# Kernel tuning notes

Measured on AMD Instinct MI355X. Metric: run time of the kernel, lower is better.

## Reference

```python
import jax, jax.numpy as jnp
import numpy as np

B = 1024
N_CPGS = 20000
N_FREQS = N_CPGS // 2 + 1  # 10001
HIDDEN = (256, 128, 64)
LN_EPS = 1e-5


def setup_inputs() -> dict:
    key = jax.random.key(0)
    keys = jax.random.split(key, 16)
    inp = {"x": jax.random.normal(keys[0], (B, N_CPGS), dtype=jnp.float32)}
    in_dim = N_FREQS
    for i, h in enumerate(HIDDEN):
        inp[f"W{i}"] = jax.random.normal(keys[1 + i], (h, in_dim), dtype=jnp.float32) * 0.01
        inp[f"alpha{i}"] = jnp.full((h, in_dim), 0.01, dtype=jnp.float32)
        inp[f"b{i}"] = jnp.zeros((h,), dtype=jnp.float32)
        inp[f"eta{i}"] = jnp.asarray(0.1, dtype=jnp.float32)
        inp[f"g{i}"] = jnp.ones((h,), dtype=jnp.float32)   # LayerNorm gamma
        inp[f"be{i}"] = jnp.zeros((h,), dtype=jnp.float32)  # LayerNorm beta
        in_dim = h
    inp["head_w"] = jax.random.normal(keys[10], (1, in_dim), dtype=jnp.float32) * (1.0 / np.sqrt(in_dim))
    inp["head_b"] = jnp.zeros((1,), dtype=jnp.float32)
    return inp


def _hebbian_layer(x, W, alpha, b, eta):
    # y_slow = x W^T + b;  plastic[b,i] = eta * tanh(y_slow)[b,i] * sum_j sigmoid(alpha)[i,j] * x_norm[b,j] * x[b,j]
    y_slow = jnp.einsum('bd,hd->bh', x, W) + b
    x_norm = x / (jnp.linalg.norm(x, axis=-1, keepdims=True) + 1e-8)
    c = x_norm * x  # (B, in) -- collapses the (B,out,in) outer-product trace algebraically
    plastic = eta * jnp.tanh(y_slow) * jnp.einsum('bd,hd->bh', c, jax.nn.sigmoid(alpha))
    return y_slow + plastic


def _layer_norm(h, g, be):
    mu = jnp.mean(h, axis=-1, keepdims=True)
    var = jnp.mean((h - mu) ** 2, axis=-1, keepdims=True)
    return (h - mu) * jax.lax.rsqrt(var + LN_EPS) * g + be


def reference(x, W0, alpha0, b0, eta0, g0, be0,
              W1, alpha1, b1, eta1, g1, be1,
              W2, alpha2, b2, eta2, g2, be2,
              head_w, head_b):
    # FFT spectral front-end
    xc = x - jnp.mean(x, axis=1, keepdims=True)
    h = jnp.log1p(jnp.abs(jnp.fft.rfft(xc, axis=1)))  # (B, N_FREQS)
    params = [(W0, alpha0, b0, eta0, g0, be0),
              (W1, alpha1, b1, eta1, g1, be1),
              (W2, alpha2, b2, eta2, g2, be2)]
    for (W, a, b, eta, g, be) in params:
        h = jax.nn.gelu(_layer_norm(_hebbian_layer(h, W, a, b, eta), g, be), approximate=False)
        # dropout is identity in eval mode
    return (jnp.einsum('bd,od->bo', h, head_w) + head_b)[:, 0]  # (B,)
```

## Files before the change

kernel.cpp:

```cpp
#include <hip/hip_runtime.h>
#include <hip/hip_bf16.h>
#include <math.h>

typedef short bf16x8 __attribute__((ext_vector_type(8)));
typedef float f32x4 __attribute__((ext_vector_type(4)));

static __device__ __forceinline__ unsigned short f2bf(float f) {
    unsigned int u = __float_as_uint(f);
    unsigned int r = (u + 0x7fffu + ((u >> 16) & 1u)) >> 16;
    return (unsigned short)r;
}

static __device__ __forceinline__ float gelu_f(float x) {
    return 0.5f * x * (1.f + erff(x * 0.70710678118654752f));
}

static __device__ __forceinline__ void gload_lds16(const void* g, void* l) {
    __builtin_amdgcn_global_load_lds(
        (const __attribute__((address_space(1))) unsigned int*)g,
        (__attribute__((address_space(3))) unsigned int*)l, 16, 0, 0);
}

static __device__ __forceinline__ int ldsmap(int i) { return i + (i >> 6); }

static __device__ __forceinline__ int rev4(int k) {
    int d0 = k % 10; k /= 10;
    int d1 = k % 10; k /= 10;
    int d2 = k % 10; int d3 = k / 10;
    return d0 * 1000 + d1 * 100 + d2 * 10 + d3;
}

static __device__ __forceinline__ void dft5(
    float a0r, float a0i, float a1r, float a1i, float a2r, float a2i,
    float a3r, float a3i, float a4r, float a4i,
    float* Xr, float* Xi)
{
    const float c1 = 0.30901699437494742f, c2 = -0.80901699437494745f;
    const float s1 = 0.95105651629515357f, s2 = 0.58778525229247312f;
    float t1r = a1r + a4r, t1i = a1i + a4i;
    float d1r = a1r - a4r, d1i = a1i - a4i;
    float t2r = a2r + a3r, t2i = a2i + a3i;
    float d2r = a2r - a3r, d2i = a2i - a3i;
    Xr[0] = a0r + t1r + t2r; Xi[0] = a0i + t1i + t2i;
    float m1r = a0r + c1 * t1r + c2 * t2r, m1i = a0i + c1 * t1i + c2 * t2i;
    float m2r = a0r + c2 * t1r + c1 * t2r, m2i = a0i + c2 * t1i + c1 * t2i;
    float n1r = s1 * d1r + s2 * d2r, n1i = s1 * d1i + s2 * d2i;
    float n2r = s2 * d1r - s1 * d2r, n2i = s2 * d1i - s1 * d2i;
    Xr[1] = m1r + n1i; Xi[1] = m1i - n1r;
    Xr[4] = m1r - n1i; Xi[4] = m1i + n1r;
    Xr[2] = m2r + n2i; Xi[2] = m2i - n2r;
    Xr[3] = m2r - n2i; Xi[3] = m2i + n2r;
}

__global__ __launch_bounds__(512, 4)
void fft_kernel(const float* __restrict__ x,
                unsigned short* __restrict__ hb,
                unsigned short* __restrict__ cb)
{
    __shared__ float reb[10156];
    __shared__ float imb[10156];
    __shared__ float redbuf[8];

    const int b = blockIdx.x;
    const int tid = threadIdx.x;
    const int lane = tid & 63;
    const int wv = tid >> 6;
    const float* xr = x + (size_t)b * 20000;

    float sum = 0.f;
    for (int i4 = tid; i4 < 5000; i4 += 512) {
        float4 v = ((const float4*)xr)[i4];
        sum += v.x + v.y + v.z + v.w;
        int n = i4 * 2;
        reb[ldsmap(n)]     = v.x; imb[ldsmap(n)]     = v.y;
        reb[ldsmap(n + 1)] = v.z; imb[ldsmap(n + 1)] = v.w;
    }
    #pragma unroll
    for (int o = 32; o; o >>= 1) sum += __shfl_xor(sum, o);
    __syncthreads();
    if (lane == 0) redbuf[wv] = sum;
    __syncthreads();
    float tot = 0.f;
    #pragma unroll
    for (int i = 0; i < 8; ++i) tot += redbuf[i];
    const float mean = tot * (1.f / 20000.f);

    const float WR[5] = {1.f, 0.80901699437494745f, 0.30901699437494742f,
                         -0.30901699437494742f, -0.80901699437494745f};
    const float WI[5] = {0.f, -0.58778525229247312f, -0.95105651629515357f,
                         -0.95105651629515357f, -0.58778525229247312f};

    #pragma unroll
    for (int s = 0; s < 4; ++s) {
        const int L  = (s == 0) ? 1000 : (s == 1) ? 100 : (s == 2) ? 10 : 1;
        const int sc = (s == 0) ? 1 : (s == 1) ? 10 : (s == 2) ? 100 : 1000;
        const float mm = (s == 0) ? mean : 0.f;
        for (int w = tid; w < 1000; w += 512) {
            const int g = w / L;
            const int j = w - g * L;
            const int base = g * (10 * L) + j;
            float ar[10], ai[10];
            #pragma unroll
            for (int u = 0; u < 10; ++u) {
                int idx = ldsmap(base + u * L);
                ar[u] = reb[idx] - mm;
                ai[u] = imb[idx] - mm;
            }
            float Er[5], Ei[5], Or[5], Oi[5];
            dft5(ar[0], ai[0], ar[2], ai[2], ar[4], ai[4], ar[6], ai[6], ar[8], ai[8], Er, Ei);
            dft5(ar[1], ai[1], ar[3], ai[3], ar[5], ai[5], ar[7], ai[7], ar[9], ai[9], Or, Oi);
            #pragma unroll
            for (int k = 1; k < 5; ++k) {
                float tr = Or[k] * WR[k] - Oi[k] * WI[k];
                Oi[k] = Or[k] * WI[k] + Oi[k] * WR[k];
                Or[k] = tr;
            }
            const float ang = (float)(j * sc) * -6.28318530717958648e-4f;
            float w1c, w1s;
            __sincosf(ang, &w1s, &w1c);
            float twr[10], twi[10];
            twr[0] = 1.f; twi[0] = 0.f;
            #pragma unroll
            for (int t = 1; t < 10; ++t) {
                twr[t] = twr[t - 1] * w1c - twi[t - 1] * w1s;
                twi[t] = twr[t - 1] * w1s + twi[t - 1] * w1c;
            }
            #pragma unroll
            for (int k = 0; k < 5; ++k) {
                float xr0 = Er[k] + Or[k], xi0 = Ei[k] + Oi[k];
                float xr1 = Er[k] - Or[k], xi1 = Ei[k] - Oi[k];
                int i0 = ldsmap(base + k * L);
                int i1 = ldsmap(base + (k + 5) * L);
                if (k == 0) {
                    reb[i0] = xr0;
                    imb[i0] = xi0;
                } else {
                    reb[i0] = xr0 * twr[k] - xi0 * twi[k];
                    imb[i0] = xr0 * twi[k] + xi0 * twr[k];
                }
                reb[i1] = xr1 * twr[k + 5] - xi1 * twi[k + 5];
                imb[i1] = xr1 * twi[k + 5] + xi1 * twr[k + 5];
            }
        }
        __syncthreads();
    }

    float harr[20];
    float sumsq = 0.f;
    unsigned short* hrow = hb + (size_t)b * 10240;
    #pragma unroll
    for (int i = 0; i < 20; ++i) {
        int k = tid + i * 512;
        float hval = 0.f;
        if (k <= 10000) {
            int k1 = (k == 10000) ? 0 : k;
            int k2 = (10000 - k) % 10000;
            int i1 = ldsmap(rev4(k1));
            int i2 = ldsmap(rev4(k2));
            float zr = reb[i1], zi = imb[i1];
            float wr = reb[i2], wi = imb[i2];
            float er = 0.5f * (zr + wr);
            float ei = 0.5f * (zi - wi);
            float odr = 0.5f * (zi + wi);
            float odi = -0.5f * (zr - wr);
            float ct, st;
            __sincosf((float)k * -3.14159265358979324e-4f, &st, &ct);
            float xre = er + ct * odr - st * odi;
            float xim = ei + ct * odi + st * odr;
            hval = log1pf(sqrtf(xre * xre + xim * xim));
        }
        harr[i] = hval;
        hrow[k] = f2bf(hval);
        sumsq += hval * hval;
    }
    #pragma unroll
    for (int o = 32; o; o >>= 1) sumsq += __shfl_xor(sumsq, o);
    __syncthreads();
    if (lane == 0) redbuf[wv] = sumsq;
    __syncthreads();
    float tsq = 0.f;
    #pragma unroll
    for (int i = 0; i < 8; ++i) tsq += redbuf[i];
    const float inv = 1.f / (sqrtf(tsq) + 1e-8f);

    unsigned short* crow = cb + (size_t)b * 10240;
    #pragma unroll
    for (int i = 0; i < 20; ++i) {
        int k = tid + i * 512;
        crow[k] = f2bf(harr[i] * harr[i] * inv);
    }
}

__global__ __launch_bounds__(256)
void prep_kernel(const float* __restrict__ W0, const float* __restrict__ A0,
                 unsigned short* __restrict__ Wb, unsigned short* __restrict__ Sb,
                 const float* __restrict__ W1, const float* __restrict__ A1,
                 const float* __restrict__ W2, const float* __restrict__ A2,
                 float* __restrict__ W1T, float* __restrict__ S1T,
                 float* __restrict__ W2T, float* __restrict__ S2T)
{
    int idx = blockIdx.x * 256 + threadIdx.x;
    if (idx < 1280128) {
        const bool isW = idx < 640064;
        const int f4 = isW ? idx : idx - 640064;
        const float* src = isW ? W0 : A0;
        unsigned short* dst = isW ? Wb : Sb;
        float4 v = ((const float4*)src)[f4];
        float e[4] = {v.x, v.y, v.z, v.w};
        int flat = f4 * 4;
        int row = flat / 10001;
        int col = flat - row * 10001;
        #pragma unroll
        for (int i = 0; i < 4; ++i) {
            if (col == 10001) { row++; col = 0; }
            float val = isW ? e[i] : 1.f / (1.f + expf(-e[i]));
            dst[(size_t)row * 10240 + col] = f2bf(val);
            col++;
        }
    } else if (idx < 1341312) {
        int i = idx - 1280128;
        int row = i / 239;
        int col = 10001 + (i - row * 239);
        Wb[(size_t)row * 10240 + col] = 0;
        Sb[(size_t)row * 10240 + col] = 0;
    } else if (idx < 1423232) {
        int o = idx - 1341312;
        if (o < 32768) {
            int d = o >> 7, h = o & 127;
            W1T[o] = W1[h * 256 + d];
        } else if (o < 65536) {
            int p = o - 32768;
            int d = p >> 7, h = p & 127;
            S1T[p] = 1.f / (1.f + expf(-A1[h * 256 + d]));
        } else if (o < 73728) {
            int p = o - 65536;
            int d = p >> 6, h = p & 63;
            W2T[p] = W2[h * 128 + d];
        } else {
            int p = o - 73728;
            int d = p >> 6, h = p & 63;
            S2T[p] = 1.f / (1.f + expf(-A2[h * 128 + d]));
        }
    }
}

__global__ __launch_bounds__(256, 2)
void gemm0_kernel(const unsigned short* __restrict__ hb, const unsigned short* __restrict__ cb,
                  const unsigned short* __restrict__ Wb, const unsigned short* __restrict__ Sb,
                  float* __restrict__ Py, float* __restrict__ Pp)
{
    __shared__ unsigned short Ah[128 * 64];
    __shared__ unsigned short Ac[128 * 64];
    __shared__ unsigned short Bw[64 * 64];
    __shared__ unsigned short Bs[64 * 64];

    const int t = threadIdx.x;
    const int b0 = blockIdx.x * 128;
    const int n0 = blockIdx.y * 64;
    const int z = blockIdx.z;
    const int lane = t & 63;
    const int wv = t >> 6;
    const int ml = lane & 15;
    const int q4 = lane >> 4;
    const int s0 = q4 ^ (ml & 7);

    const int sub = lane >> 3;
    const int sl = lane & 7;
    const int gsw = sl ^ sub;

    f32x4 accY[2][4], accP[2][4];
    #pragma unroll
    for (int mt = 0; mt < 2; ++mt)
        #pragma unroll
        for (int nt = 0; nt < 4; ++nt) {
            accY[mt][nt] = (f32x4){0.f, 0.f, 0.f, 0.f};
            accP[mt][nt] = (f32x4){0.f, 0.f, 0.f, 0.f};
        }

    const int kbase = z * 640;

    for (int step = 0; step < 10; ++step) {
        const int k0 = kbase + step * 64;
        __syncthreads();
        #pragma unroll
        for (int j = 0; j < 4; ++j) {
            const int c = wv * 4 + j;
            const size_t go = (size_t)(b0 + c * 8 + sub) * 10240 + k0 + gsw * 8;
            gload_lds16(&hb[go], &Ah[c * 512]);
            gload_lds16(&cb[go], &Ac[c * 512]);
        }
        #pragma unroll
        for (int j = 0; j < 2; ++j) {
            const int c = wv * 2 + j;
            const size_t go = (size_t)(n0 + c * 8 + sub) * 10240 + k0 + gsw * 8;
            gload_lds16(&Wb[go], &Bw[c * 512]);
            gload_lds16(&Sb[go], &Bs[c * 512]);
        }
        __syncthreads();

        #pragma unroll
        for (int kk = 0; kk < 2; ++kk) {
            const int slot = (s0 ^ (kk << 2)) << 3;
            bf16x8 ah[2], ac[2], bw[4], bs[4];
            #pragma unroll
            for (int mt = 0; mt < 2; ++mt) {
                int mrow = wv * 32 + mt * 16 + ml;
                ah[mt] = *(const bf16x8*)&Ah[mrow * 64 + slot];
                ac[mt] = *(const bf16x8*)&Ac[mrow * 64 + slot];
            }
            #pragma unroll
            for (int nt = 0; nt < 4; ++nt) {
                int nrow = nt * 16 + ml;
                bw[nt] = *(const bf16x8*)&Bw[nrow * 64 + slot];
                bs[nt] = *(const bf16x8*)&Bs[nrow * 64 + slot];
            }
            #pragma unroll
            for (int mt = 0; mt < 2; ++mt)
                #pragma unroll
                for (int nt = 0; nt < 4; ++nt) {
                    accY[mt][nt] = __builtin_amdgcn_mfma_f32_16x16x32_bf16(ah[mt], bw[nt], accY[mt][nt], 0, 0, 0);
                    accP[mt][nt] = __builtin_amdgcn_mfma_f32_16x16x32_bf16(ac[mt], bs[nt], accP[mt][nt], 0, 0, 0);
                }
        }
    }

    const int rq = q4 * 4;
    #pragma unroll
    for (int mt = 0; mt < 2; ++mt)
        #pragma unroll
        for (int nt = 0; nt < 4; ++nt)
            #pragma unroll
            for (int r = 0; r < 4; ++r) {
                int m = b0 + wv * 32 + mt * 16 + rq + r;
                int n = n0 + nt * 16 + ml;
                size_t o = ((size_t)z * 1024 + m) * 256 + n;
                Py[o] = accY[mt][nt][r];
                Pp[o] = accP[mt][nt][r];
            }
}

__global__ __launch_bounds__(256)
void combine0_kernel(const float* __restrict__ Py, const float* __restrict__ Pp,
                     const float* __restrict__ b0v, const float* __restrict__ eta0p,
                     const float* __restrict__ g0, const float* __restrict__ be0,
                     float* __restrict__ h1, float* __restrict__ c1)
{
    __shared__ float red[4];
    const int b = blockIdx.x;
    const int h = threadIdx.x;
    const int lane = h & 63;
    const int wv = h >> 6;

    float ys = 0.f, ps = 0.f;
    for (int s = 0; s < 16; ++s) {
        size_t o = ((size_t)s * 1024 + b) * 256 + h;
        ys += Py[o];
        ps += Pp[o];
    }
    float y = ys + b0v[h];
    float v = y + eta0p[0] * tanhf(y) * ps;

    float s1 = v;
    #pragma unroll
    for (int o = 32; o; o >>= 1) s1 += __shfl_xor(s1, o);
    __syncthreads();
    if (lane == 0) red[wv] = s1;
    __syncthreads();
    float sum = red[0] + red[1] + red[2] + red[3];

    float s2 = v * v;
    #pragma unroll
    for (int o = 32; o; o >>= 1) s2 += __shfl_xor(s2, o);
    __syncthreads();
    if (lane == 0) red[wv] = s2;
    __syncthreads();
    float sumsq = red[0] + red[1] + red[2] + red[3];

    float mu = sum * (1.f / 256.f);
    float var = sumsq * (1.f / 256.f) - mu * mu;
    float u = (v - mu) * rsqrtf(var + 1e-5f) * g0[h] + be0[h];
    float gl = gelu_f(u);

    float s3 = gl * gl;
    #pragma unroll
    for (int o = 32; o; o >>= 1) s3 += __shfl_xor(s3, o);
    __syncthreads();
    if (lane == 0) red[wv] = s3;
    __syncthreads();
    float gsq = red[0] + red[1] + red[2] + red[3];
    float inv = 1.f / (sqrtf(gsq) + 1e-8f);

    h1[(size_t)b * 256 + h] = gl;
    c1[(size_t)b * 256 + h] = gl * gl * inv;
}

__global__ __launch_bounds__(256)
void tail_kernel(const float* __restrict__ h1, const float* __restrict__ c1,
                 const float* __restrict__ W1T, const float* __restrict__ S1T,
                 const float* __restrict__ b1, const float* __restrict__ eta1p,
                 const float* __restrict__ g1, const float* __restrict__ be1,
                 const float* __restrict__ W2T, const float* __restrict__ S2T,
                 const float* __restrict__ b2, const float* __restrict__ eta2p,
                 const float* __restrict__ g2, const float* __restrict__ be2,
                 const float* __restrict__ hw, const float* __restrict__ hbod,
                 float* __restrict__ out)
{
    __shared__ float sh[8][256];
    __shared__ float sc[8][256];
    __shared__ float sv[8][128];
    __shared__ float sh2[8][128];
    __shared__ float sc2[8][128];
    __shared__ float sv2[8][64];

    const int t = threadIdx.x;
    const int b0 = blockIdx.x * 8;
    const int lane = t & 63;
    const int wv = t >> 6;

    #pragma unroll
    for (int i = 0; i < 8; ++i) {
        int idx = t + i * 256;
        int r = idx >> 8, d = idx & 255;
        sh[r][d] = h1[(size_t)(b0 + r) * 256 + d];
        sc[r][d] = c1[(size_t)(b0 + r) * 256 + d];
    }
    __syncthreads();

    const int hcol = t & 127;
    const int r2 = t >> 7;
    float ya[4] = {0.f, 0.f, 0.f, 0.f};
    float pa[4] = {0.f, 0.f, 0.f, 0.f};
    for (int d = 0; d < 256; ++d) {
        float w = W1T[d * 128 + hcol];
        float s = S1T[d * 128 + hcol];
        #pragma unroll
        for (int i = 0; i < 4; ++i) {
            int r = r2 * 4 + i;
            ya[i] += sh[r][d] * w;
            pa[i] += sc[r][d] * s;
        }
    }
    const float e1 = eta1p[0];
    #pragma unroll
    for (int i = 0; i < 4; ++i) {
        int r = r2 * 4 + i;
        float y = ya[i] + b1[hcol];
        sv[r][hcol] = y + e1 * tanhf(y) * pa[i];
    }
    __syncthreads();

    #pragma unroll
    for (int rr = 0; rr < 2; ++rr) {
        int r = wv * 2 + rr;
        float v0 = sv[r][lane];
        float v1 = sv[r][lane + 64];
        float s = v0 + v1, sq = v0 * v0 + v1 * v1;
        #pragma unroll
        for (int o = 32; o; o >>= 1) { s += __shfl_xor(s, o); sq += __shfl_xor(sq, o); }
        float mu = s * (1.f / 128.f);
        float var = sq * (1.f / 128.f) - mu * mu;
        float rs = rsqrtf(var + 1e-5f);
        float u0 = (v0 - mu) * rs * g1[lane] + be1[lane];
        float u1 = (v1 - mu) * rs * g1[lane + 64] + be1[lane + 64];
        float ge0 = gelu_f(u0);
        float ge1 = gelu_f(u1);
        float gsq = ge0 * ge0 + ge1 * ge1;
        #pragma unroll
        for (int o = 32; o; o >>= 1) gsq += __shfl_xor(gsq, o);
        float inv = 1.f / (sqrtf(gsq) + 1e-8f);
        sh2[r][lane] = ge0; sh2[r][lane + 64] = ge1;
        sc2[r][lane] = ge0 * ge0 * inv; sc2[r][lane + 64] = ge1 * ge1 * inv;
    }
    __syncthreads();

    const int h2c = t & 63;
    const int r4 = t >> 6;
    float yb[2] = {0.f, 0.f};
    float pb[2] = {0.f, 0.f};
    for (int d = 0; d < 128; ++d) {
        float w = W2T[d * 64 + h2c];
        float s = S2T[d * 64 + h2c];
        #pragma unroll
        for (int i = 0; i < 2; ++i) {
            int r = r4 * 2 + i;
            yb[i] += sh2[r][d] * w;
            pb[i] += sc2[r][d] * s;
        }
    }
    const float e2 = eta2p[0];
    #pragma unroll
    for (int i = 0; i < 2; ++i) {
        int r = r4 * 2 + i;
        float y = yb[i] + b2[h2c];
        sv2[r][h2c] = y + e2 * tanhf(y) * pb[i];
    }
    __syncthreads();

    #pragma unroll
    for (int rr = 0; rr < 2; ++rr) {
        int r = wv * 2 + rr;
        float v0 = sv2[r][lane];
        float s = v0, sq = v0 * v0;
        #pragma unroll
        for (int o = 32; o; o >>= 1) { s += __shfl_xor(s, o); sq += __shfl_xor(sq, o); }
        float mu = s * (1.f / 64.f);
        float var = sq * (1.f / 64.f) - mu * mu;
        float rs = rsqrtf(var + 1e-5f);
        float u = (v0 - mu) * rs * g2[lane] + be2[lane];
        float g = gelu_f(u);
        float hc = g * hw[lane];
        #pragma unroll
        for (int o = 32; o; o >>= 1) hc += __shfl_xor(hc, o);
        if (lane == 0) out[b0 + r] = hc + hbod[0];
    }
}

extern "C" void kernel_launch(void* const* d_in, const int* in_sizes, int n_in,
                              void* d_out, int out_size, void* d_ws, size_t ws_size,
                              hipStream_t stream)
{
    const float* x    = (const float*)d_in[0];
    const float* W0   = (const float*)d_in[1];
    const float* A0   = (const float*)d_in[2];
    const float* b0   = (const float*)d_in[3];
    const float* eta0 = (const float*)d_in[4];
    const float* g0   = (const float*)d_in[5];
    const float* be0  = (const float*)d_in[6];
    const float* W1   = (const float*)d_in[7];
    const float* A1   = (const float*)d_in[8];
    const float* b1   = (const float*)d_in[9];
    const float* eta1 = (const float*)d_in[10];
    const float* g1   = (const float*)d_in[11];
    const float* be1  = (const float*)d_in[12];
    const float* W2   = (const float*)d_in[13];
    const float* A2   = (const float*)d_in[14];
    const float* b2   = (const float*)d_in[15];
    const float* eta2 = (const float*)d_in[16];
    const float* g2   = (const float*)d_in[17];
    const float* be2  = (const float*)d_in[18];
    const float* hw   = (const float*)d_in[19];
    const float* hbod = (const float*)d_in[20];
    float* out = (float*)d_out;

    char* w = (char*)d_ws;
    unsigned short* hb  = (unsigned short*)(w + 0);
    unsigned short* cb  = (unsigned short*)(w + 20971520);
    unsigned short* Wb0 = (unsigned short*)(w + 41943040);
    unsigned short* Sb0 = (unsigned short*)(w + 47185920);
    float* Py  = (float*)(w + 52428800);
    float* Pp  = (float*)(w + 69206016);
    float* h1  = (float*)(w + 85983232);
    float* c1  = (float*)(w + 87031808);
    float* W1T = (float*)(w + 88080384);
    float* S1T = (float*)(w + 88211456);
    float* W2T = (float*)(w + 88342528);
    float* S2T = (float*)(w + 88375296);

    hipLaunchKernelGGL(fft_kernel, dim3(1024), dim3(512), 0, stream, x, hb, cb);
    hipLaunchKernelGGL(prep_kernel, dim3(5560), dim3(256), 0, stream,
                       W0, A0, Wb0, Sb0, W1, A1, W2, A2, W1T, S1T, W2T, S2T);
    hipLaunchKernelGGL(gemm0_kernel, dim3(8, 4, 16), dim3(256), 0, stream, hb, cb, Wb0, Sb0, Py, Pp);
    hipLaunchKernelGGL(combine0_kernel, dim3(1024), dim3(256), 0, stream, Py, Pp, b0, eta0, g0, be0, h1, c1);
    hipLaunchKernelGGL(tail_kernel, dim3(128), dim3(256), 0, stream, h1, c1, W1T, S1T, b1, eta1, g1, be1,
                       W2T, S2T, b2, eta2, g2, be2, hw, hbod, out);
}
```

Before: 295.7 us.

## Fuse FFT and weight-prep kernels, specialize FFT stages, halve tail rows per block

Merges the FFT front-end and the weight conversion/transpose prep into one launch, with blocks beyond the first 1024 doing prep work. The radix-10 stages become templated so the mean subtraction, index division and last-stage twiddles are resolved at compile time. The tail kernel now handles 4 rows per block across 256 blocks instead of 8 rows across 128, which spreads the small MLP over more CUs. The prep blocks request the same 80KB of LDS as the FFT blocks, which may limit how many can be resident at once.

Result: faster. 281.9 us (-4.7%).

```diff
diff --git a/kernel.cpp b/kernel.cpp
--- a/kernel.cpp
+++ b/kernel.cpp
@@ -52,70 +52,50 @@
     Xr[3] = m2r - n2i; Xi[3] = m2i + n2r;
 }
 
-__global__ __launch_bounds__(512, 4)
-void fft_kernel(const float* __restrict__ x,
-                unsigned short* __restrict__ hb,
-                unsigned short* __restrict__ cb)
-{
-    __shared__ float reb[10156];
-    __shared__ float imb[10156];
-    __shared__ float redbuf[8];
-
-    const int b = blockIdx.x;
-    const int tid = threadIdx.x;
-    const int lane = tid & 63;
-    const int wv = tid >> 6;
-    const float* xr = x + (size_t)b * 20000;
-
-    float sum = 0.f;
-    for (int i4 = tid; i4 < 5000; i4 += 512) {
-        float4 v = ((const float4*)xr)[i4];
-        sum += v.x + v.y + v.z + v.w;
-        int n = i4 * 2;
-        reb[ldsmap(n)]     = v.x; imb[ldsmap(n)]     = v.y;
-        reb[ldsmap(n + 1)] = v.z; imb[ldsmap(n + 1)] = v.w;
-    }
-    #pragma unroll
-    for (int o = 32; o; o >>= 1) sum += __shfl_xor(sum, o);
-    __syncthreads();
-    if (lane == 0) redbuf[wv] = sum;
-    __syncthreads();
-    float tot = 0.f;
-    #pragma unroll
-    for (int i = 0; i < 8; ++i) tot += redbuf[i];
-    const float mean = tot * (1.f / 20000.f);
+template<int S>
+static __device__ __forceinline__ void radix10_stage(
+    float* __restrict__ reb, float* __restrict__ imb, int tid, float mean)
+{
+    constexpr int L  = (S == 0) ? 1000 : (S == 1) ? 100 : (S == 2) ? 10 : 1;
+    constexpr int SC = (S == 0) ? 1 : (S == 1) ? 10 : (S == 2) ? 100 : 1000;
+    constexpr bool TW = (S != 3);
 
     const float WR[5] = {1.f, 0.80901699437494745f, 0.30901699437494742f,
                          -0.30901699437494742f, -0.80901699437494745f};
     const float WI[5] = {0.f, -0.58778525229247312f, -0.95105651629515357f,
                          -0.95105651629515357f, -0.58778525229247312f};
 
-    #pragma unroll
-    for (int s = 0; s < 4; ++s) {
-        const int L  = (s == 0) ? 1000 : (s == 1) ? 100 : (s == 2) ? 10 : 1;
-        const int sc = (s == 0) ? 1 : (s == 1) ? 10 : (s == 2) ? 100 : 1000;
-        const float mm = (s == 0) ? mean : 0.f;
-        for (int w = tid; w < 1000; w += 512) {
-            const int g = w / L;
-            const int j = w - g * L;
-            const int base = g * (10 * L) + j;
-            float ar[10], ai[10];
-            #pragma unroll
-            for (int u = 0; u < 10; ++u) {
-                int idx = ldsmap(base + u * L);
-                ar[u] = reb[idx] - mm;
-                ai[u] = imb[idx] - mm;
-            }
-            float Er[5], Ei[5], Or[5], Oi[5];
-            dft5(ar[0], ai[0], ar[2], ai[2], ar[4], ai[4], ar[6], ai[6], ar[8], ai[8], Er, Ei);
-            dft5(ar[1], ai[1], ar[3], ai[3], ar[5], ai[5], ar[7], ai[7], ar[9], ai[9], Or, Oi);
-            #pragma unroll
-            for (int k = 1; k < 5; ++k) {
-                float tr = Or[k] * WR[k] - Oi[k] * WI[k];
-                Oi[k] = Or[k] * WI[k] + Oi[k] * WR[k];
-                Or[k] = tr;
-            }
-            const float ang = (float)(j * sc) * -6.28318530717958648e-4f;
+    for (int w = tid; w < 1000; w += 512) {
+        int g, j;
+        if (S == 0)      { g = 0; j = w; }
+        else if (S == 3) { g = w; j = 0; }
+        else             { g = w / L; j = w - g * L; }
+        const int base = g * (10 * L) + j;
+
+        float ar[10], ai[10];
+        #pragma unroll
+        for (int u = 0; u < 10; ++u) {
+            int idx = ldsmap(base + u * L);
+            ar[u] = reb[idx];
+            ai[u] = imb[idx];
+        }
+        if (S == 0) {
+            #pragma unroll
+            for (int u = 0; u < 10; ++u) { ar[u] -= mean; ai[u] -= mean; }
+        }
+
+        float Er[5], Ei[5], Or[5], Oi[5];
+        dft5(ar[0], ai[0], ar[2], ai[2], ar[4], ai[4], ar[6], ai[6], ar[8], ai[8], Er, Ei);
+        dft5(ar[1], ai[1], ar[3], ai[3], ar[5], ai[5], ar[7], ai[7], ar[9], ai[9], Or, Oi);
+        #pragma unroll
+        for (int k = 1; k < 5; ++k) {
+            float tr = Or[k] * WR[k] - Oi[k] * WI[k];
+            Oi[k] = Or[k] * WI[k] + Oi[k] * WR[k];
+            Or[k] = tr;
+        }
+
+        if (TW) {
+            const float ang = (float)(j * SC) * -6.28318530717958648e-4f;
             float w1c, w1s;
             __sincosf(ang, &w1s, &w1c);
             float twr[10], twi[10];
@@ -141,9 +121,112 @@
                 reb[i1] = xr1 * twr[k + 5] - xi1 * twi[k + 5];
                 imb[i1] = xr1 * twi[k + 5] + xi1 * twr[k + 5];
             }
-        }
-        __syncthreads();
-    }
+        } else {
+            #pragma unroll
+            for (int k = 0; k < 5; ++k) {
+                int i0 = ldsmap(base + k * L);
+                int i1 = ldsmap(base + (k + 5) * L);
+                reb[i0] = Er[k] + Or[k]; imb[i0] = Ei[k] + Oi[k];
+                reb[i1] = Er[k] - Or[k]; imb[i1] = Ei[k] - Oi[k];
+            }
+        }
+    }
+}
+
+__global__ __launch_bounds__(512, 4)
+void fft_prep_kernel(const float* __restrict__ x,
+                     unsigned short* __restrict__ hb,
+                     unsigned short* __restrict__ cb,
+                     const float* __restrict__ W0, const float* __restrict__ A0,
+                     unsigned short* __restrict__ Wb, unsigned short* __restrict__ Sb,
+                     const float* __restrict__ W1, const float* __restrict__ A1,
+                     const float* __restrict__ W2, const float* __restrict__ A2,
+                     float* __restrict__ W1T, float* __restrict__ S1T,
+                     float* __restrict__ W2T, float* __restrict__ S2T)
+{
+    if (blockIdx.x >= 1024) {
+        int idx = (blockIdx.x - 1024) * 512 + threadIdx.x;
+        if (idx < 1280128) {
+            const bool isW = idx < 640064;
+            const int f4 = isW ? idx : idx - 640064;
+            const float* src = isW ? W0 : A0;
+            unsigned short* dst = isW ? Wb : Sb;
+            float4 v = ((const float4*)src)[f4];
+            float e[4] = {v.x, v.y, v.z, v.w};
+            int flat = f4 * 4;
+            int row = flat / 10001;
+            int col = flat - row * 10001;
+            #pragma unroll
+            for (int i = 0; i < 4; ++i) {
+                if (col == 10001) { row++; col = 0; }
+                float val = isW ? e[i] : 1.f / (1.f + expf(-e[i]));
+                dst[(size_t)row * 10240 + col] = f2bf(val);
+                col++;
+            }
+        } else if (idx < 1341312) {
+            int i = idx - 1280128;
+            int row = i / 239;
+            int col = 10001 + (i - row * 239);
+            Wb[(size_t)row * 10240 + col] = 0;
+            Sb[(size_t)row * 10240 + col] = 0;
+        } else if (idx < 1423232) {
+            int o = idx - 1341312;
+            if (o < 32768) {
+                int d = o >> 7, h = o & 127;
+                W1T[o] = W1[h * 256 + d];
+            } else if (o < 65536) {
+                int p = o - 32768;
+                int d = p >> 7, h = p & 127;
+                S1T[p] = 1.f / (1.f + expf(-A1[h * 256 + d]));
+            } else if (o < 73728) {
+                int p = o - 65536;
+                int d = p >> 6, h = p & 63;
+                W2T[p] = W2[h * 128 + d];
+            } else {
+                int p = o - 73728;
+                int d = p >> 6, h = p & 63;
+                S2T[p] = 1.f / (1.f + expf(-A2[h * 128 + d]));
+            }
+        }
+        return;
+    }
+
+    __shared__ float reb[10156];
+    __shared__ float imb[10156];
+    __shared__ float redbuf[8];
+
+    const int b = blockIdx.x;
+    const int tid = threadIdx.x;
+    const int lane = tid & 63;
+    const int wv = tid >> 6;
+    const float* xr = x + (size_t)b * 20000;
+
+    float sum = 0.f;
+    for (int i4 = tid; i4 < 5000; i4 += 512) {
+        float4 v = ((const float4*)xr)[i4];
+        sum += v.x + v.y + v.z + v.w;
+        int n = i4 * 2;
+        reb[ldsmap(n)]     = v.x; imb[ldsmap(n)]     = v.y;
+        reb[ldsmap(n + 1)] = v.z; imb[ldsmap(n + 1)] = v.w;
+    }
+    #pragma unroll
+    for (int o = 32; o; o >>= 1) sum += __shfl_xor(sum, o);
+    __syncthreads();
+    if (lane == 0) redbuf[wv] = sum;
+    __syncthreads();
+    float tot = 0.f;
+    #pragma unroll
+    for (int i = 0; i < 8; ++i) tot += redbuf[i];
+    const float mean = tot * (1.f / 20000.f);
+
+    radix10_stage<0>(reb, imb, tid, mean);
+    __syncthreads();
+    radix10_stage<1>(reb, imb, tid, 0.f);
+    __syncthreads();
+    radix10_stage<2>(reb, imb, tid, 0.f);
+    __syncthreads();
+    radix10_stage<3>(reb, imb, tid, 0.f);
+    __syncthreads();
 
     float harr[20];
     float sumsq = 0.f;
@@ -191,59 +274,6 @@
     }
 }
 
-__global__ __launch_bounds__(256)
-void prep_kernel(const float* __restrict__ W0, const float* __restrict__ A0,
-                 unsigned short* __restrict__ Wb, unsigned short* __restrict__ Sb,
-                 const float* __restrict__ W1, const float* __restrict__ A1,
-                 const float* __restrict__ W2, const float* __restrict__ A2,
-                 float* __restrict__ W1T, float* __restrict__ S1T,
-                 float* __restrict__ W2T, float* __restrict__ S2T)
-{
-    int idx = blockIdx.x * 256 + threadIdx.x;
-    if (idx < 1280128) {
-        const bool isW = idx < 640064;
-        const int f4 = isW ? idx : idx - 640064;
-        const float* src = isW ? W0 : A0;
-        unsigned short* dst = isW ? Wb : Sb;
-        float4 v = ((const float4*)src)[f4];
-        float e[4] = {v.x, v.y, v.z, v.w};
-        int flat = f4 * 4;
-        int row = flat / 10001;
-        int col = flat - row * 10001;
-        #pragma unroll
-        for (int i = 0; i < 4; ++i) {
-            if (col == 10001) { row++; col = 0; }
-            float val = isW ? e[i] : 1.f / (1.f + expf(-e[i]));
-            dst[(size_t)row * 10240 + col] = f2bf(val);
-            col++;
-        }
-    } else if (idx < 1341312) {
-        int i = idx - 1280128;
-        int row = i / 239;
-        int col = 10001 + (i - row * 239);
-        Wb[(size_t)row * 10240 + col] = 0;
-        Sb[(size_t)row * 10240 + col] = 0;
-    } else if (idx < 1423232) {
-        int o = idx - 1341312;
-        if (o < 32768) {
-            int d = o >> 7, h = o & 127;
-            W1T[o] = W1[h * 256 + d];
-        } else if (o < 65536) {
-            int p = o - 32768;
-            int d = p >> 7, h = p & 127;
-            S1T[p] = 1.f / (1.f + expf(-A1[h * 256 + d]));
-        } else if (o < 73728) {
-            int p = o - 65536;
-            int d = p >> 6, h = p & 63;
-            W2T[p] = W2[h * 128 + d];
-        } else {
-            int p = o - 73728;
-            int d = p >> 6, h = p & 63;
-            S2T[p] = 1.f / (1.f + expf(-A2[h * 128 + d]));
-        }
-    }
-}
-
 __global__ __launch_bounds__(256, 2)
 void gemm0_kernel(const unsigned short* __restrict__ hb, const unsigned short* __restrict__ cb,
                   const unsigned short* __restrict__ Wb, const unsigned short* __restrict__ Sb,
@@ -405,20 +435,20 @@
                  const float* __restrict__ hw, const float* __restrict__ hbod,
                  float* __restrict__ out)
 {
-    __shared__ float sh[8][256];
-    __shared__ float sc[8][256];
-    __shared__ float sv[8][128];
-    __shared__ float sh2[8][128];
-    __shared__ float sc2[8][128];
-    __shared__ float sv2[8][64];
+    __shared__ float sh[4][256];
+    __shared__ float sc[4][256];
+    __shared__ float sv[4][128];
+    __shared__ float sh2[4][128];
+    __shared__ float sc2[4][128];
+    __shared__ float sv2[4][64];
 
     const int t = threadIdx.x;
-    const int b0 = blockIdx.x * 8;
+    const int b0 = blockIdx.x * 4;
     const int lane = t & 63;
     const int wv = t >> 6;
 
     #pragma unroll
-    for (int i = 0; i < 8; ++i) {
+    for (int i = 0; i < 4; ++i) {
         int idx = t + i * 256;
         int r = idx >> 8, d = idx & 255;
         sh[r][d] = h1[(size_t)(b0 + r) * 256 + d];
@@ -428,30 +458,29 @@
 
     const int hcol = t & 127;
     const int r2 = t >> 7;
-    float ya[4] = {0.f, 0.f, 0.f, 0.f};
-    float pa[4] = {0.f, 0.f, 0.f, 0.f};
+    float ya[2] = {0.f, 0.f};
+    float pa[2] = {0.f, 0.f};
     for (int d = 0; d < 256; ++d) {
         float w = W1T[d * 128 + hcol];
         float s = S1T[d * 128 + hcol];
         #pragma unroll
-        for (int i = 0; i < 4; ++i) {
-            int r = r2 * 4 + i;
+        for (int i = 0; i < 2; ++i) {
+            int r = r2 * 2 + i;
             ya[i] += sh[r][d] * w;
             pa[i] += sc[r][d] * s;
         }
     }
     const float e1 = eta1p[0];
     #pragma unroll
-    for (int i = 0; i < 4; ++i) {
-        int r = r2 * 4 + i;
+    for (int i = 0; i < 2; ++i) {
+        int r = r2 * 2 + i;
         float y = ya[i] + b1[hcol];
         sv[r][hcol] = y + e1 * tanhf(y) * pa[i];
     }
     __syncthreads();
 
-    #pragma unroll
-    for (int rr = 0; rr < 2; ++rr) {
-        int r = wv * 2 + rr;
+    {
+        int r = wv;
         float v0 = sv[r][lane];
         float v1 = sv[r][lane + 64];
         float s = v0 + v1, sq = v0 * v0 + v1 * v1;
@@ -475,30 +504,20 @@
 
     const int h2c = t & 63;
     const int r4 = t >> 6;
-    float yb[2] = {0.f, 0.f};
-    float pb[2] = {0.f, 0.f};
+    float yb = 0.f, pb = 0.f;
     for (int d = 0; d < 128; ++d) {
-        float w = W2T[d * 64 + h2c];
-        float s = S2T[d * 64 + h2c];
-        #pragma unroll
-        for (int i = 0; i < 2; ++i) {
-            int r = r4 * 2 + i;
-            yb[i] += sh2[r][d] * w;
-            pb[i] += sc2[r][d] * s;
-        }
-    }
-    const float e2 = eta2p[0];
-    #pragma unroll
-    for (int i = 0; i < 2; ++i) {
-        int r = r4 * 2 + i;
-        float y = yb[i] + b2[h2c];
-        sv2[r][h2c] = y + e2 * tanhf(y) * pb[i];
-    }
-    __syncthreads();
-
-    #pragma unroll
-    for (int rr = 0; rr < 2; ++rr) {
-        int r = wv * 2 + rr;
+        yb += sh2[r4][d] * W2T[d * 64 + h2c];
+        pb += sc2[r4][d] * S2T[d * 64 + h2c];
+    }
+    {
+        const float e2 = eta2p[0];
+        float y = yb + b2[h2c];
+        sv2[r4][h2c] = y + e2 * tanhf(y) * pb;
+    }
+    __syncthreads();
+
+    {
+        int r = wv;
         float v0 = sv2[r][lane];
         float s = v0, sq = v0 * v0;
         #pragma unroll
@@ -556,11 +575,10 @@
     float* W2T = (float*)(w + 88342528);
     float* S2T = (float*)(w + 88375296);
 
-    hipLaunchKernelGGL(fft_kernel, dim3(1024), dim3(512), 0, stream, x, hb, cb);
-    hipLaunchKernelGGL(prep_kernel, dim3(5560), dim3(256), 0, stream,
-                       W0, A0, Wb0, Sb0, W1, A1, W2, A2, W1T, S1T, W2T, S2T);
+    hipLaunchKernelGGL(fft_prep_kernel, dim3(3804), dim3(512), 0, stream,
+                       x, hb, cb, W0, A0, Wb0, Sb0, W1, A1, W2, A2, W1T, S1T, W2T, S2T);
     hipLaunchKernelGGL(gemm0_kernel, dim3(8, 4, 16), dim3(256), 0, stream, hb, cb, Wb0, Sb0, Py, Pp);
     hipLaunchKernelGGL(combine0_kernel, dim3(1024), dim3(256), 0, stream, Py, Pp, b0, eta0, g0, be0, h1, c1);
-    hipLaunchKernelGGL(tail_kernel, dim3(128), dim3(256), 0, stream, h1, c1, W1T, S1T, b1, eta1, g1, be1,
+    hipLaunchKernelGGL(tail_kernel, dim3(256), dim3(256), 0, stream, h1, c1, W1T, S1T, b1, eta1, g1, be1,
                        W2T, S2T, b2, eta2, g2, be2, hw, hbod, out);
 }
```
